# Optimization experiments

Hardware: AMD Instinct MI355X
Metric: run time of the kernel (lower is better)

## Reference

```python
import jax, jax.numpy as jnp
import numpy as np

B, H, L, D = 8, 8, 2048, 64
FACTOR = 5


def _num_sel(length):
    return min(int(FACTOR * np.ceil(np.log(length))), length)


def setup_inputs() -> dict:
    key = jax.random.key(0)
    kq, kk, kv, ki = jax.random.split(key, 4)
    num_k = _num_sel(L)
    return {
        "q": jax.random.normal(kq, (B, H, L, D), dtype=jnp.float32),
        "k": jax.random.normal(kk, (B, H, L, D), dtype=jnp.float32),
        "v": jax.random.normal(kv, (B, H, L, D), dtype=jnp.float32),
        "random_index": jax.random.randint(ki, (L, num_k), 0, L, dtype=jnp.int32),
    }


def reference(q, k, v, random_index):
    b, h, q_len, d = q.shape
    k_len = k.shape[2]
    num_q = _num_sel(q_len)

    # --- random K sampling per query: k_s[b,h,i,j,:] = k[b,h,random_index[i,j],:]
    k_s = k[:, :, random_index, :]                      # (B,H,L,num_k,D)
    pre_attn = jnp.einsum('bhid,bhijd->bhij', q, k_s)   # (B,H,L,num_k)
    measure = pre_attn.max(-1) - pre_attn.sum(-1) / k_len  # (B,H,L)

    # --- top-k query selection (sorted=False in torch; order-insensitive math)
    _, idx = jax.lax.top_k(measure, num_q)              # (B,H,num_q)
    q_sel = jnp.take_along_axis(q, idx[..., None], axis=2)  # (B,H,num_q,D)

    # --- reduced attention over all keys
    attn = jnp.einsum('bhid,bhjd->bhij', q_sel, k) * (d ** -0.5)  # (B,H,num_q,k_len)

    # ProbMask: causal mask per selected query index (mask where j > idx[i])
    mask = jnp.arange(k_len)[None, None, None, :] > idx[..., None]
    attn = jnp.where(mask, -jnp.inf, attn)
    attn = jax.nn.softmax(attn, axis=-1)

    out_sel = jnp.einsum('bhij,bhjd->bhid', attn, v)    # (B,H,num_q,D)

    # --- context initialization (use_mask=True branch) and scatter back
    context = jnp.cumsum(v, axis=2)                     # (B,H,L,D)
    bi = jnp.arange(b)[:, None, None]
    hi = jnp.arange(h)[None, :, None]
    out = context.at[bi, hi, idx].set(out_sel)          # (B,H,L,D)
    return out, attn
```

## Files before the change

kernel.cpp:

```cpp
#include <hip/hip_runtime.h>
#include <float.h>
#include <math.h>

#define B_  8
#define H_  8
#define L_  2048
#define D_  64
#define NS  40
#define BH  (B_*H_)
#define SCALE 0.125f


template<int CTRL>
__device__ __forceinline__ float dpp_add(float x) {
    int s = __builtin_amdgcn_update_dpp(0, __float_as_int(x), CTRL, 0xF, 0xF, true);
    return x + __int_as_float(s);
}

__global__ __launch_bounds__(256) void measure_cumsum_kernel(
    const float* __restrict__ q, const float* __restrict__ k,
    const int* __restrict__ ridx, float* __restrict__ measure,
    const float* __restrict__ v, float* __restrict__ out)
{
    __shared__ float4 part[64][5];
    if (blockIdx.x < 256) {
        int b = blockIdx.x;
        int xcd = b & 7, s = b >> 3;
        int bh  = xcd + ((s >> 2) << 3);
        int cg  = s & 3;
        int col = threadIdx.x & 3, sub = threadIdx.x >> 2;
        int c0 = cg*4 + col;
        int r0 = sub * 32;
        const float4* vb = (const float4*)(v + (size_t)bh * L_ * D_);
        float4*       ob = (float4*)(out + (size_t)bh * L_ * D_);

        float4 acc = make_float4(0,0,0,0);
        #pragma unroll
        for (int r = 0; r < 32; ++r) {
            float4 x = vb[(size_t)(r0 + r)*16 + c0];
            acc.x += x.x; acc.y += x.y; acc.z += x.z; acc.w += x.w;
        }
        part[sub][col] = acc;
        __syncthreads();

        float4 run = make_float4(0,0,0,0);
        for (int cc = 0; cc < sub; ++cc) {
            float4 x = part[cc][col];
            run.x += x.x; run.y += x.y; run.z += x.z; run.w += x.w;
        }

        #pragma unroll
        for (int r = 0; r < 32; ++r) {
            float4 x = vb[(size_t)(r0 + r)*16 + c0];
            run.x += x.x; run.y += x.y; run.z += x.z; run.w += x.w;
            ob[(size_t)(r0 + r)*16 + c0] = run;
        }
        return;
    }
    int wave = threadIdx.x >> 6, lane = threadIdx.x & 63;
    int b = blockIdx.x - 256;
    int xcd = b & 7, s = b >> 3;
    int bh  = xcd + ((s >> 9) << 3);
    int i   = (s & 511) * 4 + wave;
    int oct = lane >> 3;
    int e   = lane & 7;

    int4 r4 = *(const int4*)(ridx + i * NS + oct * 4);
    int  r5 = ridx[i * NS + 32 + oct];
    int rr[5] = { r4.x, r4.y, r4.z, r4.w, r5 };

    const float4* kb = (const float4*)(k + (size_t)bh * L_ * D_);
    const float4* qp = (const float4*)(q + ((size_t)bh * L_ + i) * D_);
    float4 qa = qp[e];
    float4 qb = qp[e + 8];

    float mx = -FLT_MAX, sm = 0.f;
    #pragma unroll
    for (int p = 0; p < 5; ++p) {
        int base = rr[p] << 4;
        float4 ka = kb[base + e];
        float4 kc = kb[base + 8 + e];
        float pa = qa.x*ka.x + qa.y*ka.y + qa.z*ka.z + qa.w*ka.w;
        float pb = qb.x*kc.x + qb.y*kc.y + qb.z*kc.z + qb.w*kc.w;
        float pp = pa + pb;
        pp = dpp_add<0x111>(pp);
        pp = dpp_add<0x112>(pp);
        pp = dpp_add<0x114>(pp);
        mx = fmaxf(mx, pp);
        sm += pp;
    }
    mx = fmaxf(mx, __shfl_xor(mx,  8, 64));  sm += __shfl_xor(sm,  8, 64);
    mx = fmaxf(mx, __shfl_xor(mx, 16, 64));  sm += __shfl_xor(sm, 16, 64);
    mx = fmaxf(mx, __shfl_xor(mx, 32, 64));  sm += __shfl_xor(sm, 32, 64);
    if (lane == 7)
        measure[(size_t)bh * L_ + i] = mx - sm * (1.0f / (float)L_);
}

__global__ __launch_bounds__(256) void topk_kernel(
    const float* __restrict__ measure, int* __restrict__ idxOut)
{
    __shared__ float segVal[4][NS];
    __shared__ int   segIdx[4][NS];
    int bh = blockIdx.x;
    int t = threadIdx.x, w = t >> 6, lane = t & 63;
    const float4* m4 = (const float4*)(measure + (size_t)bh * L_);

    float vals[8];
    float4 a  = m4[128*w + 2*lane];
    float4 bb = m4[128*w + 2*lane + 1];
    vals[0]=a.x;  vals[1]=a.y;  vals[2]=a.z;  vals[3]=a.w;
    vals[4]=bb.x; vals[5]=bb.y; vals[6]=bb.z; vals[7]=bb.w;
    int gbase = 512*w + 8*lane;

    float lv = -FLT_MAX; int li = 0x7fffffff;
    #pragma unroll
    for (int e = 0; e < 8; ++e)
        if (vals[e] > lv) { lv = vals[e]; li = gbase + e; }

    for (int r = 0; r < NS; ++r) {
        float v = lv; int idx = li;
        #pragma unroll
        for (int off = 32; off; off >>= 1) {
            float ov = __shfl_xor(v, off, 64);
            int   oi = __shfl_xor(idx, off, 64);
            if (ov > v || (ov == v && oi < idx)) { v = ov; idx = oi; }
        }
        if (lane == 0) { segVal[w][r] = v; segIdx[w][r] = idx; }
        if (((idx >> 3) & 63) == lane) {
            int slot = idx & 7;
            #pragma unroll
            for (int e = 0; e < 8; ++e) if (e == slot) vals[e] = -FLT_MAX;
            lv = -FLT_MAX; li = 0x7fffffff;
            #pragma unroll
            for (int e = 0; e < 8; ++e)
                if (vals[e] > lv) { lv = vals[e]; li = gbase + e; }
        }
    }
    __syncthreads();

    if (w == 0) {
        int s = lane & 3;
        int h = 0;
        float hv = segVal[s][0]; int hi_ = segIdx[s][0];
        for (int r = 0; r < NS; ++r) {
            float v = hv; int idx = hi_; int ws = s;
            float ov = __shfl_xor(v, 1, 64); int oi = __shfl_xor(idx, 1, 64); int os = __shfl_xor(ws, 1, 64);
            if (ov > v || (ov == v && oi < idx)) { v = ov; idx = oi; ws = os; }
            ov = __shfl_xor(v, 2, 64); oi = __shfl_xor(idx, 2, 64); os = __shfl_xor(ws, 2, 64);
            if (ov > v || (ov == v && oi < idx)) { v = ov; idx = oi; ws = os; }
            if (lane == 0) idxOut[bh*NS + r] = idx;
            if (s == ws) {
                ++h;
                if (h < NS) { hv = segVal[s][h]; hi_ = segIdx[s][h]; }
                else        { hv = -FLT_MAX;     hi_ = 0x7fffffff;  }
            }
        }
    }
}

__global__ __launch_bounds__(256) void scores_kernel(
    const float* __restrict__ q, const float* __restrict__ k,
    const int* __restrict__ idxSel, float* __restrict__ attn)
{
    __shared__ float4 kbuf[16 * 129];
    int b = blockIdx.x;
    int xcd = b & 7, s = b >> 3;
    int bh  = xcd + ((s / 10) << 3);
    int grp = s % 10;
    int qi = threadIdx.x >> 6, sub = threadIdx.x & 63;
    int rank = grp*4 + qi;
    int qrow = idxSel[bh*NS + rank];

    const float4* qrp = (const float4*)(q + ((size_t)bh * L_ + qrow) * D_);
    float4 qreg[16];
    #pragma unroll
    for (int g = 0; g < 16; ++g) qreg[g] = qrp[g];

    const float4* kb = (const float4*)(k + (size_t)bh * L_ * D_);
    float sc0[16], sc1[16];

    #pragma unroll
    for (int c = 0; c < 16; ++c) {
        __syncthreads();
        int j0 = c * 128;
        #pragma unroll
        for (int it = 0; it < 8; ++it) {
            int fi = threadIdx.x + 256*it;
            int g = fi & 15, j = fi >> 4;
            kbuf[g*129 + j] = kb[(size_t)(j0 + j)*16 + g];
        }
        __syncthreads();
        float acc0 = 0.f, acc1 = 0.f;
        #pragma unroll
        for (int g = 0; g < 16; ++g) {
            float4 k0 = kbuf[g*129 + sub];
            float4 k1 = kbuf[g*129 + sub + 64];
            float4 qq = qreg[g];
            acc0 += qq.x*k0.x + qq.y*k0.y + qq.z*k0.z + qq.w*k0.w;
            acc1 += qq.x*k1.x + qq.y*k1.y + qq.z*k1.z + qq.w*k1.w;
        }
        sc0[c] = acc0 * SCALE;
        sc1[c] = acc1 * SCALE;
    }

    float mx = -FLT_MAX;
    #pragma unroll
    for (int c = 0; c < 16; ++c) {
        if (c*128 + sub      <= qrow) mx = fmaxf(mx, sc0[c]);
        if (c*128 + sub + 64 <= qrow) mx = fmaxf(mx, sc1[c]);
    }
    #pragma unroll
    for (int off = 32; off; off >>= 1) mx = fmaxf(mx, __shfl_xor(mx, off, 64));

    float sum = 0.f;
    #pragma unroll
    for (int c = 0; c < 16; ++c) {
        sc0[c] = (c*128 + sub      <= qrow) ? __expf(sc0[c] - mx) : 0.f;
        sc1[c] = (c*128 + sub + 64 <= qrow) ? __expf(sc1[c] - mx) : 0.f;
        sum += sc0[c] + sc1[c];
    }
    #pragma unroll
    for (int off = 32; off; off >>= 1) sum += __shfl_xor(sum, off, 64);
    float inv = 1.f / sum;

    float* arow = attn + (size_t)(bh*NS + rank) * L_;
    #pragma unroll
    for (int c = 0; c < 16; ++c) {
        arow[c*128 + sub]      = sc0[c] * inv;
        arow[c*128 + sub + 64] = sc1[c] * inv;
    }
}

__global__ __launch_bounds__(256) void pv_kernel(
    const float* __restrict__ v, const int* __restrict__ idxSel,
    const float* __restrict__ attn, float* __restrict__ out)
{
    __shared__ float wl[4][L_ + 64];
    __shared__ float4 part[16][16];
    __shared__ int qr4[4];
    int b = blockIdx.x;
    int xcd = b & 7, s = b >> 3;
    int bh  = xcd + ((s / 10) << 3);
    int grp = s % 10;
    int t = threadIdx.x;
    if (t < 4) qr4[t] = idxSel[bh*NS + grp*4 + t];

    #pragma unroll
    for (int it = 0; it < 8; ++it) {
        int f = t + 256*it;
        int rr = f >> 9, fi = f & 511;
        const float4* ar = (const float4*)(attn + (size_t)(bh*NS + grp*4 + rr) * L_);
        float4 x = ar[fi];
        int j = 4*fi;
        *((float4*)&wl[rr][j + 4*(j >> 7)]) = x;
    }
    __syncthreads();

    int maxq = max(max(qr4[0], qr4[1]), max(qr4[2], qr4[3]));
    int d4 = t & 15, seg = t >> 4;
    const float4* vb = (const float4*)(v + (size_t)bh * L_ * D_);
    float4 acc[4];
    #pragma unroll
    for (int rr = 0; rr < 4; ++rr) acc[rr] = make_float4(0,0,0,0);

    int jlo = seg*128, jhi = min(jlo + 127, maxq);
    for (int j = jlo; j <= jhi; ++j) {
        float4 x = vb[(size_t)j*16 + d4];
        int jp = j + 4*(j >> 7);
        #pragma unroll
        for (int rr = 0; rr < 4; ++rr) {
            float wgt = wl[rr][jp];
            acc[rr].x += wgt*x.x; acc[rr].y += wgt*x.y;
            acc[rr].z += wgt*x.z; acc[rr].w += wgt*x.w;
        }
    }

    #pragma unroll
    for (int rr = 0; rr < 4; ++rr) {
        part[seg][d4] = acc[rr];
        __syncthreads();
        float4 a = acc[rr];
        for (int s2 = 8; s2; s2 >>= 1) {
            if (seg < s2) {
                float4 o = part[seg + s2][d4];
                a.x += o.x; a.y += o.y; a.z += o.z; a.w += o.w;
                part[seg][d4] = a;
            }
            __syncthreads();
        }
        if (seg == 0) {
            float4* orow = (float4*)(out + ((size_t)bh * L_ + qr4[rr]) * D_);
            orow[d4] = a;
        }
        __syncthreads();
    }
}

extern "C" void kernel_launch(void* const* d_in, const int* in_sizes, int n_in,
                              void* d_out, int out_size, void* d_ws, size_t ws_size,
                              hipStream_t stream) {
    const float* q    = (const float*)d_in[0];
    const float* k    = (const float*)d_in[1];
    const float* v    = (const float*)d_in[2];
    const int*   ridx = (const int*)d_in[3];

    float* out     = (float*)d_out;
    float* attnOut = out + (size_t)BH * L_ * D_;

    float*  measure = (float*)d_ws;
    int*    idxSel  = (int*)((char*)d_ws + (size_t)BH * L_ * sizeof(float));

    measure_cumsum_kernel<<<256 + BH * L_ / 4, 256, 0, stream>>>(
        q, k, ridx, measure, v, out);
    topk_kernel   <<<BH,          256, 0, stream>>>(measure, idxSel);
    scores_kernel <<<BH * 10,     256, 0, stream>>>(q, k, idxSel, attnOut);
    pv_kernel     <<<BH * 10,     256, 0, stream>>>(v, idxSel, attnOut, out);
}
```

Baseline: 321.5 us.

## Sort selected queries by row so score blocks skip fully masked key chunks

```diff
diff --git a/kernel.cpp b/kernel.cpp
--- a/kernel.cpp
+++ b/kernel.cpp
@@ -142,19 +142,29 @@
         int s = lane & 3;
         int h = 0;
         float hv = segVal[s][0]; int hi_ = segIdx[s][0];
+        int myQrow = 0x7fffffff;
         for (int r = 0; r < NS; ++r) {
             float v = hv; int idx = hi_; int ws = s;
             float ov = __shfl_xor(v, 1, 64); int oi = __shfl_xor(idx, 1, 64); int os = __shfl_xor(ws, 1, 64);
             if (ov > v || (ov == v && oi < idx)) { v = ov; idx = oi; ws = os; }
             ov = __shfl_xor(v, 2, 64); oi = __shfl_xor(idx, 2, 64); os = __shfl_xor(ws, 2, 64);
             if (ov > v || (ov == v && oi < idx)) { v = ov; idx = oi; ws = os; }
-            if (lane == 0) idxOut[bh*NS + r] = idx;
+            if (lane == r) myQrow = idx;
             if (s == ws) {
                 ++h;
                 if (h < NS) { hv = segVal[s][h]; hi_ = segIdx[s][h]; }
                 else        { hv = -FLT_MAX;     hi_ = 0x7fffffff;  }
             }
         }
+        int pos = 0;
+        for (int j = 0; j < NS; ++j) {
+            int qj = __shfl(myQrow, j, 64);
+            if (lane < NS && qj < myQrow) ++pos;
+        }
+        if (lane >= NS) pos = lane;
+        int packed = (lane << 16) | (myQrow & 0xffff);
+        int sorted = __builtin_amdgcn_ds_permute(pos << 2, packed);
+        if (lane < NS) idxOut[bh*NS + lane] = sorted;
     }
 }
 
@@ -163,13 +173,20 @@
     const int* __restrict__ idxSel, float* __restrict__ attn)
 {
     __shared__ float4 kbuf[16 * 129];
+    __shared__ int qpk[4];
     int b = blockIdx.x;
     int xcd = b & 7, s = b >> 3;
     int bh  = xcd + ((s / 10) << 3);
     int grp = s % 10;
     int qi = threadIdx.x >> 6, sub = threadIdx.x & 63;
-    int rank = grp*4 + qi;
-    int qrow = idxSel[bh*NS + rank];
+    int packed = idxSel[bh*NS + grp*4 + qi];
+    int qrow = packed & 0xffff;
+    int rank = packed >> 16;
+
+    if (sub == 0) qpk[qi] = qrow;
+    __syncthreads();
+    int maxq = max(max(qpk[0], qpk[1]), max(qpk[2], qpk[3]));
+    int cmax = (maxq >> 7) + 1;
 
     const float4* qrp = (const float4*)(q + ((size_t)bh * L_ + qrow) * D_);
     float4 qreg[16];
@@ -178,9 +195,10 @@
 
     const float4* kb = (const float4*)(k + (size_t)bh * L_ * D_);
     float sc0[16], sc1[16];
-
-    #pragma unroll
-    for (int c = 0; c < 16; ++c) {
+    #pragma unroll
+    for (int c = 0; c < 16; ++c) { sc0[c] = 0.f; sc1[c] = 0.f; }
+
+    for (int c = 0; c < cmax; ++c) {
         __syncthreads();
         int j0 = c * 128;
         #pragma unroll
@@ -238,18 +256,24 @@
     __shared__ float wl[4][L_ + 64];
     __shared__ float4 part[16][16];
     __shared__ int qr4[4];
+    __shared__ int rk4[4];
     int b = blockIdx.x;
     int xcd = b & 7, s = b >> 3;
     int bh  = xcd + ((s / 10) << 3);
     int grp = s % 10;
     int t = threadIdx.x;
-    if (t < 4) qr4[t] = idxSel[bh*NS + grp*4 + t];
+    if (t < 4) {
+        int p = idxSel[bh*NS + grp*4 + t];
+        qr4[t] = p & 0xffff;
+        rk4[t] = p >> 16;
+    }
+    __syncthreads();
 
     #pragma unroll
     for (int it = 0; it < 8; ++it) {
         int f = t + 256*it;
         int rr = f >> 9, fi = f & 511;
-        const float4* ar = (const float4*)(attn + (size_t)(bh*NS + grp*4 + rr) * L_);
+        const float4* ar = (const float4*)(attn + (size_t)(bh*NS + rk4[rr]) * L_);
         float4 x = ar[fi];
         int j = 4*fi;
         *((float4*)&wl[rr][j + 4*(j >> 7)]) = x;
```

New measurement: 326.1 us. About the same (+1.4%).
